# Optimization experiments

Measured on AMD Instinct MI355X. Metric: run time of the kernel, lower is better.

## Reference

```python
import jax, jax.numpy as jnp
import numpy as np

D = 1024
H = 16
DEPTH = D // H


def setup_inputs() -> dict:
    key = jax.random.key(0)
    ks = jax.random.split(key, 10)
    B, S = 4, 2048
    scale = 1.0 / np.sqrt(D)
    x = jax.random.normal(ks[0], (B, S, D), dtype=jnp.float32)
    attention_mask = jnp.ones((B, S, S), dtype=jnp.int32)
    Wq = jax.random.normal(ks[1], (D, D), dtype=jnp.float32) * scale
    bq = jnp.zeros((D,), dtype=jnp.float32)
    Wk = jax.random.normal(ks[2], (D, D), dtype=jnp.float32) * scale
    bk = jnp.zeros((D,), dtype=jnp.float32)
    Wv = jax.random.normal(ks[3], (D, D), dtype=jnp.float32) * scale
    bv = jnp.zeros((D,), dtype=jnp.float32)
    Wo = jax.random.normal(ks[4], (D, D), dtype=jnp.float32) * scale
    bo = jnp.zeros((D,), dtype=jnp.float32)
    return {"x": x, "attention_mask": attention_mask,
            "Wq": Wq, "bq": bq, "Wk": Wk, "bk": bk,
            "Wv": Wv, "bv": bv, "Wo": Wo, "bo": bo}


def _split_heads(t):
    # [b, s, h*d] -> [b, h, s, d]
    b, s, _ = t.shape
    return t.reshape(b, s, H, DEPTH).transpose(0, 2, 1, 3)


def reference(x, attention_mask, Wq, bq, Wk, bk, Wv, bv, Wo, bo):
    # QKV projections (torch Linear: x @ W.T + b; here W stored as [in, out])
    q = _split_heads(x @ Wq + bq)  # [b, h, s, d]
    k = _split_heads(x @ Wk + bk)
    v = _split_heads(x @ Wv + bv)
    scores = jnp.einsum('bhsd,bhtd->bhst', q, k) / jnp.sqrt(jnp.float32(DEPTH))
    mask = attention_mask[:, None, :, :]  # [b, 1, s, s]
    scores = jnp.where(mask == 0, jnp.float32(-jnp.inf), scores)
    attn = jax.nn.softmax(scores, axis=-1)
    # Dropout is identity in eval mode
    out = jnp.einsum('bhst,bhtd->bhsd', attn, v)  # [b, h, s, d]
    b, h, s, d = out.shape
    out = out.transpose(0, 2, 1, 3).reshape(b, s, h * d)
    return out @ Wo + bo
```

## Files before the change

### kernel.cpp

```cpp
#include <hip/hip_runtime.h>
#include <hip/hip_bf16.h>

typedef __bf16 bf16;
typedef __bf16 bf16x4 __attribute__((ext_vector_type(4)));
typedef __bf16 bf16x8 __attribute__((ext_vector_type(8)));
typedef float f32x4 __attribute__((ext_vector_type(4)));

#define AS1 __attribute__((address_space(1)))
#define AS3 __attribute__((address_space(3)))

__device__ __forceinline__ void gload_lds16(const void* g, void* l) {
  __builtin_amdgcn_global_load_lds((const AS1 void*)g, (AS3 void*)l, 16, 0, 0);
}

__device__ __forceinline__ float fexp2(float x) {
#if __has_builtin(__builtin_amdgcn_exp2f)
  return __builtin_amdgcn_exp2f(x);
#else
  return exp2f(x);
#endif
}

#define BB 4
#define SS 2048
#define DD 1024
#define HH 16
#define MM (BB*SS)
#define LDQ 3072
#define NT (SS/64)
#define QSCALE 0.18033688011112042f

__global__ __launch_bounds__(256) void prep(
    const float* __restrict__ x, bf16* __restrict__ xb,
    const float* __restrict__ Wq, const float* __restrict__ Wk,
    const float* __restrict__ Wv, const float* __restrict__ Wo,
    bf16* __restrict__ WtQKV, bf16* __restrict__ Wto,
    const float* __restrict__ bq, const float* __restrict__ bk,
    const float* __restrict__ bv, float* __restrict__ ball,
    int* __restrict__ flag) {
  __shared__ float t[64][65];
  const int bid = blockIdx.x;
  if (bid < 1024) {
    int id = bid;
    int which = id >> 8;
    int bi = (id >> 4) & 15, bj = id & 15;
    const float* W = which == 0 ? Wq : which == 1 ? Wk : which == 2 ? Wv : Wo;
    bf16* Wt = which < 3 ? WtQKV + (size_t)which * 1024 * DD : Wto;
    const float scale = (which == 0) ? QSCALE : 1.0f;
    for (int c = 0; c < 16; c++) {
      int idx = threadIdx.x + c * 256;
      int r = idx >> 6, col = idx & 63;
      t[r][col] = W[(size_t)(bi * 64 + r) * DD + bj * 64 + col];
    }
    __syncthreads();
    for (int c = 0; c < 16; c++) {
      int idx = threadIdx.x + c * 256;
      int rn = idx >> 6, ck = idx & 63;
      Wt[(size_t)(bj * 64 + rn) * DD + bi * 64 + ck] = (bf16)(t[ck][rn] * scale);
    }
  } else if (bid < 5120) {
    int i = ((bid - 1024) * 256 + threadIdx.x) * 8;
    float4 a = *(const float4*)&x[i];
    float4 b = *(const float4*)&x[i + 4];
    bf16x8 o;
    o[0] = (bf16)a.x; o[1] = (bf16)a.y; o[2] = (bf16)a.z; o[3] = (bf16)a.w;
    o[4] = (bf16)b.x; o[5] = (bf16)b.y; o[6] = (bf16)b.z; o[7] = (bf16)b.w;
    *(bf16x8*)&xb[i] = o;
  } else {
    int i = (bid - 5120) * 256 + threadIdx.x;
    if (i == 0) *flag = 1;
    float v = (i < 1024) ? bq[i] * QSCALE
                         : ((i < 2048) ? bk[i - 1024] : bv[i - 2048]);
    ball[i] = v;
  }
}

template <int MODE>
__global__ __launch_bounds__(256) void gemm_bt(const bf16* __restrict__ A,
                                               const bf16* __restrict__ Bt,
                                               const float* __restrict__ bias,
                                               void* __restrict__ Cout, int ldc,
                                               bf16* __restrict__ Vt,
                                               const int4* __restrict__ mask4,
                                               int* __restrict__ flag) {
  constexpr int K = 1024;
  constexpr int BM = 128, BN = 128, BK = 64;
  __shared__ bf16 As[BM * BK];
  __shared__ bf16 Bs[BN * BK];
  const int tid = threadIdx.x;
  const int w = tid >> 6, l = tid & 63;
  const int wm = w >> 1, wn = w & 1;
  const int by = blockIdx.x, bx = blockIdx.y;

  f32x4 acc[4][4] = {};

  const int sRow = l >> 3;
  const int sSlot = (l & 7) ^ sRow;
  const bf16* aBase = A + (size_t)(by * BM + w * 32 + sRow) * K + sSlot * 8;
  const bf16* bBase = Bt + (size_t)(bx * BN + w * 32 + sRow) * K + sSlot * 8;

  const int n4 = BB * SS * SS / 4;
  int mi = (by * 24 + bx) * 256 + tid;
  int ok = 1;
  int kiter = 0;

  for (int k0 = 0; k0 < K; k0 += BK) {
    int4 mv = {1, 1, 1, 1};
    bool have = (MODE == 2) && (kiter < 11) && (mi < n4);
    if (have) mv = mask4[mi];

    #pragma unroll
    for (int c = 0; c < 4; c++) {
      gload_lds16(aBase + (size_t)(c * 8) * K + k0, &As[(w * 32 + c * 8) * BK]);
      gload_lds16(bBase + (size_t)(c * 8) * K + k0, &Bs[(w * 32 + c * 8) * BK]);
    }
    __syncthreads();
    #pragma unroll
    for (int kk = 0; kk < 2; kk++) {
      bf16x8 af[4], bfr[4];
      #pragma unroll
      for (int i = 0; i < 4; i++) {
        int row = wm * 64 + i * 16 + (l & 15);
        int sl = (kk * 4 + (l >> 4)) ^ (row & 7);
        af[i] = *(const bf16x8*)(&As[row * BK + sl * 8]);
      }
      #pragma unroll
      for (int j = 0; j < 4; j++) {
        int row = wn * 64 + j * 16 + (l & 15);
        int sl = (kk * 4 + (l >> 4)) ^ (row & 7);
        bfr[j] = *(const bf16x8*)(&Bs[row * BK + sl * 8]);
      }
      #pragma unroll
      for (int i = 0; i < 4; i++)
        #pragma unroll
        for (int j = 0; j < 4; j++)
          acc[i][j] = __builtin_amdgcn_mfma_f32_16x16x32_bf16(af[i], bfr[j],
                                                              acc[i][j], 0, 0, 0);
    }
    __syncthreads();

    if (have) {
      if (!(mv.x && mv.y && mv.z && mv.w)) ok = 0;
      mi += 1536 * 256;
    }
    kiter++;
  }

  if (MODE == 2 && bx >= 16) {
    #pragma unroll
    for (int j = 0; j < 4; j++) {
      int col = bx * BN + wn * 64 + j * 16 + (l & 15);
      int n = col - 2048;
      float bb = bias[col];
      #pragma unroll
      for (int i = 0; i < 4; i++) {
        int row0 = by * BM + wm * 64 + i * 16 + (l >> 4) * 4;
        int b_ = row0 >> 11;
        int s0 = row0 & 2047;
        bf16x4 vv;
        #pragma unroll
        for (int r = 0; r < 4; r++) vv[r] = (bf16)(acc[i][j][r] + bb);
        *(bf16x4*)&Vt[(size_t)(b_ * 1024 + n) * SS + s0] = vv;
      }
    }
  } else {
    #pragma unroll
    for (int j = 0; j < 4; j++) {
      int col = bx * BN + wn * 64 + j * 16 + (l & 15);
      float bb = bias[col];
      #pragma unroll
      for (int i = 0; i < 4; i++) {
        int row0 = by * BM + wm * 64 + i * 16 + (l >> 4) * 4;
        #pragma unroll
        for (int r = 0; r < 4; r++) {
          float v = acc[i][j][r] + bb;
          if (MODE == 2)
            ((bf16*)Cout)[(size_t)(row0 + r) * ldc + col] = (bf16)v;
          else
            ((float*)Cout)[(size_t)(row0 + r) * ldc + col] = v;
        }
      }
    }
  }

  if (MODE == 2) {
    if (__ballot(!ok)) {
      if ((tid & 63) == 0) atomicAnd(flag, 0);
    }
  }
}

__global__ __launch_bounds__(256, 2) void attn_fwd(const bf16* __restrict__ QKV,
                                                   const bf16* __restrict__ Vt,
                                                   const int* __restrict__ mask,
                                                   const int* __restrict__ flag,
                                                   bf16* __restrict__ att) {
  __shared__ bf16 Ks[2][64 * 64];
  __shared__ bf16 Vs[2][64 * 64];
  const int tid = threadIdx.x, w = tid >> 6, l = tid & 63;
  const int g = l >> 4, q = l & 15;
  const int bh = blockIdx.x, b = bh >> 4, h = bh & 15;
  const int q0 = blockIdx.y * 256 + w * 64;
  const bool allones = (*flag != 0);

  bf16x8 bq[4][2];
  #pragma unroll
  for (int qb = 0; qb < 4; qb++) {
    const bf16* qptr =
        QKV + (size_t)(b * SS + q0 + qb * 16 + q) * LDQ + h * 64 + g * 8;
    bq[qb][0] = *(const bf16x8*)qptr;
    bq[qb][1] = *(const bf16x8*)(qptr + 32);
  }

  bf16x8 ones;
  #pragma unroll
  for (int j = 0; j < 8; j++) ones[j] = (bf16)1.0f;

  f32x4 o[4][4] = {};
  f32x4 ls[4] = {};

  const int sSlot = (l & 7) ^ ((l >> 3) & 7);
  const bf16* kPtr[2];
  #pragma unroll
  for (int c = 0; c < 2; c++) {
    int B8 = 2 * w + c;
    int tl = 32 * (B8 >> 2) + 16 * (B8 & 1) + 4 * ((B8 >> 1) & 1) +
             8 * (l >> 5) + ((l >> 3) & 3);
    kPtr[c] = QKV + (size_t)(b * SS + tl) * LDQ + 1024 + h * 64 + sSlot * 8;
  }
  const bf16* vBase =
      Vt + (size_t)(b * 1024 + h * 64 + w * 16 + (l >> 3)) * SS + sSlot * 8;

  gload_lds16(kPtr[0], &Ks[0][(2 * w + 0) * 8 * 64]);
  gload_lds16(kPtr[1], &Ks[0][(2 * w + 1) * 8 * 64]);
  gload_lds16(vBase, &Vs[0][(w * 16) * 64]);
  gload_lds16(vBase + (size_t)8 * SS, &Vs[0][(w * 16 + 8) * 64]);

  for (int it = 0; it < NT; ++it) {
    const int cur = it & 1;
    if (it + 1 < NT) {
      const int t1 = (it + 1) * 64;
      gload_lds16(kPtr[0] + (size_t)t1 * LDQ, &Ks[cur ^ 1][(2 * w + 0) * 8 * 64]);
      gload_lds16(kPtr[1] + (size_t)t1 * LDQ, &Ks[cur ^ 1][(2 * w + 1) * 8 * 64]);
      gload_lds16(vBase + t1, &Vs[cur ^ 1][(w * 16) * 64]);
      gload_lds16(vBase + (size_t)8 * SS + t1, &Vs[cur ^ 1][(w * 16 + 8) * 64]);
      asm volatile("s_waitcnt vmcnt(4)" ::: "memory");
    } else {
      asm volatile("s_waitcnt vmcnt(0)" ::: "memory");
    }
    __builtin_amdgcn_s_barrier();
    asm volatile("" ::: "memory");

    const bf16* ks = Ks[cur];
    const bf16* vs = Vs[cur];

    bf16x8 af[4][2];
    #pragma unroll
    for (int tt = 0; tt < 4; tt++) {
      int row = tt * 16 + q;
      af[tt][0] = *(const bf16x8*)(&ks[row * 64 + (g ^ (q & 7)) * 8]);
      af[tt][1] = *(const bf16x8*)(&ks[row * 64 + (((4 + g) ^ (q & 7))) * 8]);
    }

    bf16x8 pb[4][2];
    #pragma unroll
    for (int qb = 0; qb < 4; qb++) {
      f32x4 s4[4];
      #pragma unroll
      for (int tt = 0; tt < 4; tt++) {
        f32x4 z = {};
        z = __builtin_amdgcn_mfma_f32_16x16x32_bf16(af[tt][0], bq[qb][0], z, 0, 0, 0);
        z = __builtin_amdgcn_mfma_f32_16x16x32_bf16(af[tt][1], bq[qb][1], z, 0, 0, 0);
        s4[tt] = z;
      }

      if (!allones) {
        const int t0 = it * 64;
        #pragma unroll
        for (int tt = 0; tt < 4; tt++)
          #pragma unroll
          for (int r = 0; r < 4; r++) {
            int tl = 32 * (tt >> 1) + 8 * g + 4 * (tt & 1) + r;
            if (mask[(size_t)(b * SS + q0 + qb * 16 + q) * SS + t0 + tl] == 0)
              s4[tt][r] = -1e30f;
          }
      }

      #pragma unroll
      for (int kk = 0; kk < 2; kk++) {
        bf16x8 f;
        #pragma unroll
        for (int j = 0; j < 8; j++)
          f[j] = (bf16)fexp2(s4[2 * kk + (j >> 2)][j & 3]);
        pb[qb][kk] = f;
      }
      ls[qb] = __builtin_amdgcn_mfma_f32_16x16x32_bf16(ones, pb[qb][0], ls[qb], 0, 0, 0);
      ls[qb] = __builtin_amdgcn_mfma_f32_16x16x32_bf16(ones, pb[qb][1], ls[qb], 0, 0, 0);
    }

    __builtin_amdgcn_s_setprio(1);
    #pragma unroll
    for (int kk = 0; kk < 2; kk++) {
      int cc = kk * 4 + g;
      #pragma unroll
      for (int n = 0; n < 4; n++) {
        int vrow = n * 16 + q;
        int vsl = cc ^ (q & 7);
        bf16x8 av = *(const bf16x8*)(&vs[vrow * 64 + vsl * 8]);
        #pragma unroll
        for (int qb = 0; qb < 4; qb++)
          o[qb][n] = __builtin_amdgcn_mfma_f32_16x16x32_bf16(av, pb[qb][kk],
                                                             o[qb][n], 0, 0, 0);
      }
    }
    __builtin_amdgcn_s_setprio(0);

    asm volatile("" ::: "memory");
    __builtin_amdgcn_s_barrier();
    asm volatile("" ::: "memory");
  }

  #pragma unroll
  for (int qb = 0; qb < 4; qb++) {
    float inv = 1.0f / ls[qb][0];
    #pragma unroll
    for (int n = 0; n < 4; n++) {
      bf16x4 ov;
      #pragma unroll
      for (int r = 0; r < 4; r++) ov[r] = (bf16)(o[qb][n][r] * inv);
      *(bf16x4*)&att[(size_t)(b * SS + q0 + qb * 16 + q) * DD + h * 64 +
                     n * 16 + g * 4] = ov;
    }
  }
}

extern "C" void kernel_launch(void* const* d_in, const int* in_sizes, int n_in,
                              void* d_out, int out_size, void* d_ws, size_t ws_size,
                              hipStream_t stream) {
  const float* x = (const float*)d_in[0];
  const int* mask = (const int*)d_in[1];
  const float* Wq = (const float*)d_in[2];
  const float* bq = (const float*)d_in[3];
  const float* Wk = (const float*)d_in[4];
  const float* bk = (const float*)d_in[5];
  const float* Wv = (const float*)d_in[6];
  const float* bv = (const float*)d_in[7];
  const float* Wo = (const float*)d_in[8];
  const float* bo = (const float*)d_in[9];
  float* out = (float*)d_out;

  char* p = (char*)d_ws;
  const size_t MB16 = (size_t)MM * DD * 2;
  bf16* xb = (bf16*)p;   p += MB16;
  bf16* QKV = (bf16*)p;  p += (size_t)MM * LDQ * 2;
  bf16* Vt = (bf16*)p;   p += MB16;
  bf16* Wt_all = (bf16*)p; p += (size_t)3072 * DD * 2;
  bf16* Wot = (bf16*)p;  p += (size_t)DD * DD * 2;
  float* ball = (float*)p; p += 3072 * 4;
  int* flag = (int*)p;
  bf16* att = xb;

  prep<<<5132, 256, 0, stream>>>(x, xb, Wq, Wk, Wv, Wo, Wt_all, Wot,
                                 bq, bk, bv, ball, flag);
  gemm_bt<2><<<dim3(64, 24), 256, 0, stream>>>(xb, Wt_all, ball, QKV, LDQ,
                                               Vt, (const int4*)mask, flag);
  attn_fwd<<<dim3(BB * HH, SS / 256), 256, 0, stream>>>(QKV, Vt, mask, flag, att);
  gemm_bt<0><<<dim3(64, 8), 256, 0, stream>>>(att, Wot, bo, out, DD,
                                              Vt, (const int4*)mask, flag);
}
```

Baseline: 166.3 us.

## Replace QKV GEMM with 256x256 tiled, double-buffered 8-wave pipelined kernel

Replaces the templated QKV projection GEMM with a dedicated kernel. It uses 256x256 output tiles, 512 threads and double-buffered LDS stages loaded with global_load_lds, with the loads spread across the compute phases under explicit waitcnt and barrier control and raised priority around MFMA. Block IDs are swizzled so blocks scheduled together share L2 data, and the mask all-ones check is folded into the pipelined loop. The output GEMM becomes a plain non-templated kernel. The aim is more data reuse per tile and better overlap of memory and MFMA, at the cost of higher register and LDS use (128 KB LDS per block) and fewer blocks in the grid.

```diff
diff --git a/kernel.cpp b/kernel.cpp
--- a/kernel.cpp
+++ b/kernel.cpp
@@ -28,6 +28,7 @@
 #define MM (BB*SS)
 #define LDQ 3072
 #define NT (SS/64)
+#define NMASK4 (BB*SS*SS/4)
 #define QSCALE 0.18033688011112042f
 
 __global__ __launch_bounds__(256) void prep(
@@ -75,14 +76,155 @@
   }
 }
 
-template <int MODE>
-__global__ __launch_bounds__(256) void gemm_bt(const bf16* __restrict__ A,
-                                               const bf16* __restrict__ Bt,
-                                               const float* __restrict__ bias,
-                                               void* __restrict__ Cout, int ldc,
-                                               bf16* __restrict__ Vt,
-                                               const int4* __restrict__ mask4,
-                                               int* __restrict__ flag) {
+__global__ __launch_bounds__(512, 2) void gemm_qkv_8ph(
+    const bf16* __restrict__ A, const bf16* __restrict__ Bt,
+    const float* __restrict__ bias, bf16* __restrict__ QKV,
+    bf16* __restrict__ Vt, const int4* __restrict__ mask4,
+    int* __restrict__ flag) {
+  __shared__ bf16 lds[2][2][256 * 64];
+  const int tid = threadIdx.x;
+  const int l = tid & 63;
+  const int wid = tid >> 6, wr = wid >> 2, wc = wid & 3;
+
+  const int id = blockIdx.x;
+  const int swz = (id & 7) * 48 + (id >> 3);
+  const int by = swz / 12, bx = swz % 12;
+
+  f32x4 acc[8][4] = {};
+
+  const int r0 = tid >> 3;
+  const int se = ((tid & 7) ^ (r0 & 7)) * 8;
+  const bf16* aSrc = A + (size_t)(by * 256 + r0) * 1024 + se;
+  const bf16* bSrc = Bt + (size_t)(bx * 256 + r0) * 1024 + se;
+  const int dE = r0 * 64 + (tid & 7) * 8;
+
+  int ok = 1;
+  const int gthr = blockIdx.x * 512 + tid;
+
+#define STAGE_HT(slot, j, ht)                                                \
+  do {                                                                       \
+    const bf16* s_ = ((ht) < 2 ? aSrc : bSrc);                               \
+    const int h_ = (ht) & 1;                                                 \
+    gload_lds16(s_ + (size_t)(h_ * 128) * 1024 + (j) * 64,                   \
+                &lds[slot][(ht) >> 1][(h_ * 128) * 64 + dE]);                \
+    gload_lds16(s_ + (size_t)(h_ * 128 + 64) * 1024 + (j) * 64,              \
+                &lds[slot][(ht) >> 1][(h_ * 128 + 64) * 64 + dE]);           \
+  } while (0)
+
+  STAGE_HT(0, 0, 0); STAGE_HT(0, 0, 1); STAGE_HT(0, 0, 2); STAGE_HT(0, 0, 3);
+  STAGE_HT(1, 1, 0); STAGE_HT(1, 1, 1); STAGE_HT(1, 1, 2);
+  asm volatile("s_waitcnt vmcnt(6)" ::: "memory");
+  __builtin_amdgcn_s_barrier();
+
+  for (int j = 0; j < 16; ++j) {
+    const int s = j & 1;
+    bf16x8 bfr[4][2];
+    int4 mv0 = {1, 1, 1, 1}, mv1 = {1, 1, 1, 1};
+    bool hv0 = false, hv1 = false;
+
+    #pragma unroll
+    for (int cq = 0; cq < 4; ++cq) {
+      bf16x8 afr[2][2];
+      #pragma unroll
+      for (int m2 = 0; m2 < 2; ++m2) {
+        int row = wr * 128 + (cq * 2 + m2) * 16 + (l & 15);
+        #pragma unroll
+        for (int kk = 0; kk < 2; ++kk) {
+          int sl = (kk * 4 + (l >> 4)) ^ (l & 7);
+          afr[m2][kk] = *(const bf16x8*)(&lds[s][0][row * 64 + sl * 8]);
+        }
+      }
+      if (cq == 0) {
+        #pragma unroll
+        for (int ni = 0; ni < 4; ++ni) {
+          int row = wc * 64 + ni * 16 + (l & 15);
+          #pragma unroll
+          for (int kk = 0; kk < 2; ++kk) {
+            int sl = (kk * 4 + (l >> 4)) ^ (l & 7);
+            bfr[ni][kk] = *(const bf16x8*)(&lds[s][1][row * 64 + sl * 8]);
+          }
+        }
+        if (j <= 10) {
+          int i0 = gthr + (j * 2) * 196608;
+          int i1 = gthr + (j * 2 + 1) * 196608;
+          hv0 = i0 < NMASK4;
+          hv1 = i1 < NMASK4;
+          if (hv0) mv0 = mask4[i0];
+          if (hv1) mv1 = mask4[i1];
+        }
+        asm volatile("s_waitcnt lgkmcnt(8)" ::: "memory");
+      }
+      if (cq == 1 && j + 1 < 16) STAGE_HT((j + 1) & 1, j + 1, 3);
+
+      __builtin_amdgcn_s_barrier();
+      asm volatile("s_waitcnt lgkmcnt(0)" ::: "memory");
+      __builtin_amdgcn_s_setprio(1);
+      #pragma unroll
+      for (int kk = 0; kk < 2; ++kk)
+        #pragma unroll
+        for (int m2 = 0; m2 < 2; ++m2)
+          #pragma unroll
+          for (int ni = 0; ni < 4; ++ni)
+            acc[cq * 2 + m2][ni] = __builtin_amdgcn_mfma_f32_16x16x32_bf16(
+                afr[m2][kk], bfr[ni][kk], acc[cq * 2 + m2][ni], 0, 0, 0);
+      __builtin_amdgcn_s_setprio(0);
+
+      if (cq == 3) {
+        if (j + 2 < 16) {
+          STAGE_HT(s, j + 2, 0);
+          STAGE_HT(s, j + 2, 1);
+          STAGE_HT(s, j + 2, 2);
+          asm volatile("s_waitcnt vmcnt(6)" ::: "memory");
+        } else if (j + 1 < 16) {
+          asm volatile("s_waitcnt vmcnt(0)" ::: "memory");
+        }
+        if (hv0 && !(mv0.x && mv0.y && mv0.z && mv0.w)) ok = 0;
+        if (hv1 && !(mv1.x && mv1.y && mv1.z && mv1.w)) ok = 0;
+      }
+      __builtin_amdgcn_s_barrier();
+    }
+  }
+#undef STAGE_HT
+
+  if (bx >= 8) {
+    #pragma unroll
+    for (int ni = 0; ni < 4; ++ni) {
+      int col = bx * 256 + wc * 64 + ni * 16 + (l & 15);
+      int n = col - 2048;
+      float bb = bias[col];
+      #pragma unroll
+      for (int mi = 0; mi < 8; ++mi) {
+        int row0 = by * 256 + wr * 128 + mi * 16 + (l >> 4) * 4;
+        int b_ = row0 >> 11, s0 = row0 & 2047;
+        bf16x4 vv;
+        #pragma unroll
+        for (int r = 0; r < 4; ++r) vv[r] = (bf16)(acc[mi][ni][r] + bb);
+        *(bf16x4*)&Vt[(size_t)(b_ * 1024 + n) * SS + s0] = vv;
+      }
+    }
+  } else {
+    #pragma unroll
+    for (int ni = 0; ni < 4; ++ni) {
+      int col = bx * 256 + wc * 64 + ni * 16 + (l & 15);
+      float bb = bias[col];
+      #pragma unroll
+      for (int mi = 0; mi < 8; ++mi) {
+        int row0 = by * 256 + wr * 128 + mi * 16 + (l >> 4) * 4;
+        #pragma unroll
+        for (int r = 0; r < 4; ++r)
+          QKV[(size_t)(row0 + r) * LDQ + col] = (bf16)(acc[mi][ni][r] + bb);
+      }
+    }
+  }
+  if (__ballot(!ok)) {
+    if ((tid & 63) == 0) atomicAnd(flag, 0);
+  }
+}
+
+__global__ __launch_bounds__(256) void gemm_out(const bf16* __restrict__ A,
+                                                const bf16* __restrict__ Bt,
+                                                const float* __restrict__ bias,
+                                                float* __restrict__ Cout) {
   constexpr int K = 1024;
   constexpr int BM = 128, BN = 128, BK = 64;
   __shared__ bf16 As[BM * BK];
@@ -99,16 +241,7 @@
   const bf16* aBase = A + (size_t)(by * BM + w * 32 + sRow) * K + sSlot * 8;
   const bf16* bBase = Bt + (size_t)(bx * BN + w * 32 + sRow) * K + sSlot * 8;
 
-  const int n4 = BB * SS * SS / 4;
-  int mi = (by * 24 + bx) * 256 + tid;
-  int ok = 1;
-  int kiter = 0;
-
   for (int k0 = 0; k0 < K; k0 += BK) {
-    int4 mv = {1, 1, 1, 1};
-    bool have = (MODE == 2) && (kiter < 11) && (mi < n4);
-    if (have) mv = mask4[mi];
-
     #pragma unroll
     for (int c = 0; c < 4; c++) {
       gload_lds16(aBase + (size_t)(c * 8) * K + k0, &As[(w * 32 + c * 8) * BK]);
@@ -138,54 +271,18 @@
                                                               acc[i][j], 0, 0, 0);
     }
     __syncthreads();
-
-    if (have) {
-      if (!(mv.x && mv.y && mv.z && mv.w)) ok = 0;
-      mi += 1536 * 256;
-    }
-    kiter++;
-  }
-
-  if (MODE == 2 && bx >= 16) {
-    #pragma unroll
-    for (int j = 0; j < 4; j++) {
-      int col = bx * BN + wn * 64 + j * 16 + (l & 15);
-      int n = col - 2048;
-      float bb = bias[col];
-      #pragma unroll
-      for (int i = 0; i < 4; i++) {
-        int row0 = by * BM + wm * 64 + i * 16 + (l >> 4) * 4;
-        int b_ = row0 >> 11;
-        int s0 = row0 & 2047;
-        bf16x4 vv;
-        #pragma unroll
-        for (int r = 0; r < 4; r++) vv[r] = (bf16)(acc[i][j][r] + bb);
-        *(bf16x4*)&Vt[(size_t)(b_ * 1024 + n) * SS + s0] = vv;
-      }
-    }
-  } else {
-    #pragma unroll
-    for (int j = 0; j < 4; j++) {
-      int col = bx * BN + wn * 64 + j * 16 + (l & 15);
-      float bb = bias[col];
-      #pragma unroll
-      for (int i = 0; i < 4; i++) {
-        int row0 = by * BM + wm * 64 + i * 16 + (l >> 4) * 4;
-        #pragma unroll
-        for (int r = 0; r < 4; r++) {
-          float v = acc[i][j][r] + bb;
-          if (MODE == 2)
-            ((bf16*)Cout)[(size_t)(row0 + r) * ldc + col] = (bf16)v;
-          else
-            ((float*)Cout)[(size_t)(row0 + r) * ldc + col] = v;
-        }
-      }
-    }
-  }
-
-  if (MODE == 2) {
-    if (__ballot(!ok)) {
-      if ((tid & 63) == 0) atomicAnd(flag, 0);
+  }
+
+  #pragma unroll
+  for (int j = 0; j < 4; j++) {
+    int col = bx * BN + wn * 64 + j * 16 + (l & 15);
+    float bb = bias[col];
+    #pragma unroll
+    for (int i = 0; i < 4; i++) {
+      int row0 = by * BM + wm * 64 + i * 16 + (l >> 4) * 4;
+      #pragma unroll
+      for (int r = 0; r < 4; r++)
+        Cout[(size_t)(row0 + r) * DD + col] = acc[i][j][r] + bb;
     }
   }
 }
@@ -362,9 +459,8 @@
 
   prep<<<5132, 256, 0, stream>>>(x, xb, Wq, Wk, Wv, Wo, Wt_all, Wot,
                                  bq, bk, bv, ball, flag);
-  gemm_bt<2><<<dim3(64, 24), 256, 0, stream>>>(xb, Wt_all, ball, QKV, LDQ,
-                                               Vt, (const int4*)mask, flag);
+  gemm_qkv_8ph<<<384, 512, 0, stream>>>(xb, Wt_all, ball, QKV, Vt,
+                                        (const int4*)mask, flag);
   attn_fwd<<<dim3(BB * HH, SS / 256), 256, 0, stream>>>(QKV, Vt, mask, flag, att);
-  gemm_bt<0><<<dim3(64, 8), 256, 0, stream>>>(att, Wot, bo, out, DD,
-                                              Vt, (const int4*)mask, flag);
-}
+  gemm_out<<<dim3(64, 8), 256, 0, stream>>>(att, Wot, bo, out);
+}
```

New measurement: 195.9 us. +17.8%, slower.
